# Performance work log

Measured on AMD Instinct MI355X. Metric: run time of the kernel, lower is better.

## Reference

```python
import jax, jax.numpy as jnp
import numpy as np
import math

S, B, D, H = 2048, 2, 1024, 16
HD = D // H  # head_dim = 64


def setup_inputs() -> dict:
    key = jax.random.key(0)
    ks = jax.random.split(key, 8)
    scale = 0.02
    return {
        "query": jax.random.normal(ks[0], (S, B, D), jnp.float32),
        "key": jax.random.normal(ks[1], (S, B, D), jnp.float32),
        "value": jax.random.normal(ks[2], (S, B, D), jnp.float32),
        "mask": jax.random.randint(ks[3], (1, S, 1, 1), 0, 2, jnp.int32),
        "w_q": jax.random.normal(ks[4], (D, D), jnp.float32) * scale,
        "b_q": jnp.zeros((D,), jnp.float32),
        "w_k": jax.random.normal(ks[5], (D, D), jnp.float32) * scale,
        "b_k": jnp.zeros((D,), jnp.float32),
        "w_v": jax.random.normal(ks[6], (D, D), jnp.float32) * scale,
        "b_v": jnp.zeros((D,), jnp.float32),
    }


def reference(query, key, value, mask, w_q, b_q, w_k, b_k, w_v, b_v):
    # Linear projections (torch Linear: x @ W^T + b); inputs are (S, B, D)
    q = query @ w_q.T + b_q
    k = key @ w_k.T + b_k
    v = value @ w_v.T + b_v
    # split heads: (S, B, H, HD)
    q = q.reshape(S, B, H, HD)
    k = k.reshape(S, B, H, HD)
    v = v.reshape(S, B, H, HD)
    # scores over (query_i, key_j, batch, head)
    scores = jnp.einsum("ibhd,jbhd->ijbh", q, k) * (1.0 / math.sqrt(HD))
    # mask (1, S, 1, 1) broadcasts against (i, j, b, h); 0 => masked
    scores = jnp.where(mask == 0, -jnp.inf, scores)
    # softmax over key axis j (original: nn.Softmax(dim=1))
    attn = jax.nn.softmax(scores, axis=1)
    out = jnp.einsum("ijbh,jbhd->ibhd", attn, v)  # (S, B, H, HD)
    return out.reshape(S, B, D)
```

## Files before the change

kernel.cpp:

```cpp
#include <hip/hip_runtime.h>
#include <stdint.h>


#define S_ 2048
#define B_ 2
#define D_ 1024
#define H_ 16
#define HD_ 64
#define M_ (S_ * B_)

typedef __bf16 bf16;
typedef bf16 bf16x8 __attribute__((ext_vector_type(8)));
typedef float floatx4 __attribute__((ext_vector_type(4)));

#define QSCALE 0.18033688011112042f

__device__ __forceinline__ void async_cp16(const bf16* g, bf16* l) {
    __builtin_amdgcn_global_load_lds(
        (const __attribute__((address_space(1))) void*)g,
        (__attribute__((address_space(3))) void*)l, 16, 0, 0);
}

#define TILE_OFF(bh, tile) (((size_t)(bh) * 32 + (tile)) * 4096)

__global__ __launch_bounds__(256) void mask_scan(const int* __restrict__ mask,
                                                 int* __restrict__ pos,
                                                 int* __restrict__ cnt)
{
    __shared__ int sums[256];
    const int tid = threadIdx.x;
    int v[8], s = 0;
    #pragma unroll
    for (int j = 0; j < 8; j++) { v[j] = mask[tid * 8 + j] ? 1 : 0; s += v[j]; }
    sums[tid] = s;
    __syncthreads();
    for (int off = 1; off < 256; off <<= 1) {
        int t = (tid >= off) ? sums[tid - off] : 0;
        __syncthreads();
        sums[tid] += t;
        __syncthreads();
    }
    int base = (tid > 0) ? sums[tid - 1] : 0;
    #pragma unroll
    for (int j = 0; j < 8; j++) { pos[tid * 8 + j] = base; base += v[j]; }
    if (tid == 255) cnt[0] = sums[255];
}

__global__ __launch_bounds__(256) void cvt6(
    const float* __restrict__ x0, const float* __restrict__ x1, const float* __restrict__ x2,
    const float* __restrict__ w0, const float* __restrict__ w1, const float* __restrict__ w2,
    bf16* __restrict__ o0, bf16* __restrict__ o1, bf16* __restrict__ o2,
    bf16* __restrict__ o3, bf16* __restrict__ o4, bf16* __restrict__ o5)
{
    const int z = blockIdx.y;
    if (z >= 3 && blockIdx.x >= 512) return;
    const float* src = (z == 0) ? x0 : (z == 1) ? x1 : (z == 2) ? x2
                     : (z == 3) ? w0 : (z == 4) ? w1 : w2;
    bf16* dst = (z == 0) ? o0 : (z == 1) ? o1 : (z == 2) ? o2
              : (z == 3) ? o3 : (z == 4) ? o4 : o5;
    const size_t i = ((size_t)blockIdx.x * 256 + threadIdx.x) * 8;
    floatx4 a = *(const floatx4*)(src + i);
    floatx4 b = *(const floatx4*)(src + i + 4);
    bf16x8 v;
    #pragma unroll
    for (int j = 0; j < 4; j++) { v[j] = (bf16)a[j]; v[4 + j] = (bf16)b[j]; }
    *(bf16x8*)(dst + i) = v;
}

#define TM 128
#define TN 64
#define BK 32

__global__ __launch_bounds__(256, 4) void qkv_gemm_async(
    const bf16* __restrict__ xq, const bf16* __restrict__ xk, const bf16* __restrict__ xv,
    const bf16* __restrict__ wq, const bf16* __restrict__ wk, const bf16* __restrict__ wv,
    const float* __restrict__ bq, const float* __restrict__ bk, const float* __restrict__ bv,
    const int* __restrict__ mask, const int* __restrict__ pos,
    bf16* __restrict__ oq, bf16* __restrict__ ok, bf16* __restrict__ ov)
{
    __shared__ __align__(16) bf16 a_lds[TM * BK];
    __shared__ __align__(16) bf16 b_lds[TN * BK];

    const int fid = blockIdx.x;
    const int xcd = fid & 7;
    const int t   = fid >> 3;
    const int z   = t >> 6;
    const int u   = t & 63;
    const int m0  = ((u & 3) * 8 + xcd) * TM;
    const int n0  = (u >> 2) * TN;

    const bf16*  X  = (z == 0) ? xq : (z == 1) ? xk : xv;
    const bf16*  W  = (z == 0) ? wq : (z == 1) ? wk : wv;
    const float* Bi = (z == 0) ? bq : (z == 1) ? bk : bv;

    const int tid  = threadIdx.x;
    const int wid  = tid >> 6;
    const int lane = tid & 63;
    const int wm = wid >> 1, wn = wid & 1;
    const int lm = lane & 15, lq = lane >> 4;
    const int ksw = lq ^ ((lm >> 1) & 3);

    floatx4 acc[4][2] = {};

    for (int kt = 0; kt < D_; kt += BK) {
        __syncthreads();
        #pragma unroll
        for (int tt = 0; tt < 2; tt++) {
            const int cb = (tt * 4 + wid) * 64;
            const int c  = cb + lane;
            const int row = c >> 2, kc = (c & 3) ^ ((c >> 3) & 3);
            async_cp16(X + (size_t)(m0 + row) * D_ + kt + kc * 8, a_lds + cb * 8);
        }
        {
            const int cb = wid * 64;
            const int c  = cb + lane;
            const int row = c >> 2, kc = (c & 3) ^ ((c >> 3) & 3);
            async_cp16(W + (size_t)(n0 + row) * D_ + kt + kc * 8, b_lds + cb * 8);
        }
        __syncthreads();

        bf16x8 af[4], bf[2];
        #pragma unroll
        for (int i = 0; i < 4; i++)
            af[i] = *(const bf16x8*)(a_lds + (wm * 64 + i * 16 + lm) * 32 + ksw * 8);
        #pragma unroll
        for (int j = 0; j < 2; j++)
            bf[j] = *(const bf16x8*)(b_lds + (wn * 32 + j * 16 + lm) * 32 + ksw * 8);
        #pragma unroll
        for (int i = 0; i < 4; i++)
            #pragma unroll
            for (int j = 0; j < 2; j++)
                acc[i][j] = __builtin_amdgcn_mfma_f32_16x16x32_bf16(
                    af[i], bf[j], acc[i][j], 0, 0, 0);
    }

    #pragma unroll
    for (int j = 0; j < 2; j++) {
        const int n = n0 + wn * 32 + j * 16 + lm;
        const float bias = Bi[n];
        const int h = n >> 6, hd = n & 63;
        #pragma unroll
        for (int i = 0; i < 4; i++) {
            const int mb = m0 + wm * 64 + i * 16 + lq * 4;
            #pragma unroll
            for (int r = 0; r < 4; r++) {
                const int m = mb + r;
                const int s = m >> 1, b = m & 1;
                const float v = acc[i][j][r] + bias;
                const int bh = b * H_ + h;
                if (z == 0) {
                    oq[((size_t)bh * S_ + s) * HD_ + hd] = (bf16)(v * QSCALE);
                } else if (mask[s]) {
                    const int cs = pos[s];
                    if (z == 1) {
                        ok[TILE_OFF(bh, cs >> 6) + (hd >> 3) * 512 +
                           (cs & 63) * 8 + (hd & 7)] = (bf16)v;
                    } else {
                        ov[TILE_OFF(bh, cs >> 6) + ((cs >> 3) & 7) * 512 +
                           hd * 8 + (cs & 7)] = (bf16)v;
                    }
                }
            }
        }
    }
}

__global__ __launch_bounds__(256, 4) void attn_kernel(
    const bf16* __restrict__ qw, const bf16* __restrict__ kw, const bf16* __restrict__ vtw,
    const int* __restrict__ cnt, float* __restrict__ out)
{
    __shared__ __align__(16) bf16 p_lds[4 * 16 * 72];

    const int fid  = blockIdx.x;
    const int xcd  = fid & 7;
    const int t    = fid >> 3;
    const int bh   = (t & 3) * 8 + xcd;
    const int q0   = (t >> 2) * 64;

    const int tid  = threadIdx.x;
    const int wid  = tid >> 6;
    const int lane = tid & 63;
    const int lm = lane & 15, lq = lane >> 4;
    const int count = cnt[0];
    const int ntiles = (count + 63) >> 6;

    bf16x8 qf[2];
    {
        const bf16* qp = qw + ((size_t)bh * S_ + q0 + wid * 16 + lm) * HD_;
        qf[0] = *(const bf16x8*)(qp + lq * 8);
        qf[1] = *(const bf16x8*)(qp + 32 + lq * 8);
    }

    float lsum[4] = {0.f, 0.f, 0.f, 0.f};
    floatx4 oacc[4] = {};
    bf16* pw = p_lds + wid * 16 * 72;

    for (int tl = 0; tl < ntiles; tl++) {
        const size_t tbase = TILE_OFF(bh, tl);
        const size_t foff  = (size_t)lq * 512 + (size_t)lm * 8;

        bf16x8 kf[2][4];
        #pragma unroll
        for (int ks = 0; ks < 2; ks++)
            #pragma unroll
            for (int n = 0; n < 4; n++)
                kf[ks][n] = *(const bf16x8*)(kw + tbase + ks * 2048 + foff + n * 128);

        floatx4 sacc[4] = {};
        #pragma unroll
        for (int ks = 0; ks < 2; ks++)
            #pragma unroll
            for (int n = 0; n < 4; n++)
                sacc[n] = __builtin_amdgcn_mfma_f32_16x16x32_bf16(
                    qf[ks], kf[ks][n], sacc[n], 0, 0, 0);

        const int jb = tl * 64;
        float valf[4];
        #pragma unroll
        for (int n = 0; n < 4; n++)
            valf[n] = (jb + n * 16 + lm < count) ? 1.0f : 0.0f;
        #pragma unroll
        for (int r = 0; r < 4; r++)
            #pragma unroll
            for (int n = 0; n < 4; n++) {
                const float p = exp2f(sacc[n][r]) * valf[n];
                lsum[r] += p;
                sacc[n][r] = p;
            }

        bf16x8 vf[2][4];
        #pragma unroll
        for (int ks = 0; ks < 2; ks++)
            #pragma unroll
            for (int n = 0; n < 4; n++)
                vf[ks][n] = *(const bf16x8*)(vtw + tbase + ks * 2048 + foff + n * 128);

        #pragma unroll
        for (int r = 0; r < 4; r++)
            #pragma unroll
            for (int n = 0; n < 4; n++)
                pw[(lq * 4 + r) * 72 + n * 16 + lm] = (bf16)sacc[n][r];

        #pragma unroll
        for (int ks = 0; ks < 2; ks++) {
            bf16x8 pf = *(const bf16x8*)(pw + lm * 72 + ks * 32 + lq * 8);
            #pragma unroll
            for (int n = 0; n < 4; n++)
                oacc[n] = __builtin_amdgcn_mfma_f32_16x16x32_bf16(
                    pf, vf[ks][n], oacc[n], 0, 0, 0);
        }
    }

    float invl[4];
    #pragma unroll
    for (int r = 0; r < 4; r++) {
        float lr = lsum[r];
        lr += __shfl_xor(lr, 1);
        lr += __shfl_xor(lr, 2);
        lr += __shfl_xor(lr, 4);
        lr += __shfl_xor(lr, 8);
        invl[r] = 1.0f / lr;
    }
    const int b = bh >> 4, h = bh & 15;
    #pragma unroll
    for (int n = 0; n < 4; n++)
        #pragma unroll
        for (int r = 0; r < 4; r++) {
            const int q = q0 + wid * 16 + lq * 4 + r;
            out[((size_t)q * B_ + b) * D_ + h * 64 + n * 16 + lm] = oacc[n][r] * invl[r];
        }
}

extern "C" void kernel_launch(void* const* d_in, const int* in_sizes, int n_in,
                              void* d_out, int out_size, void* d_ws, size_t ws_size,
                              hipStream_t stream) {
    const float* xq = (const float*)d_in[0];
    const float* xk = (const float*)d_in[1];
    const float* xv = (const float*)d_in[2];
    const int*  mask = (const int*)d_in[3];
    const float* wq = (const float*)d_in[4];
    const float* bq = (const float*)d_in[5];
    const float* wk = (const float*)d_in[6];
    const float* bk = (const float*)d_in[7];
    const float* wv = (const float*)d_in[8];
    const float* bv = (const float*)d_in[9];

    const size_t NX = (size_t)M_ * D_;
    const size_t NW = (size_t)D_ * D_;
    char* ws = (char*)d_ws;
    int* cnt = (int*)ws;
    int* pos = cnt + 16;
    char* base = ws + 16384;

    bf16* xqb = (bf16*)base;
    bf16* xkb = xqb + NX;
    bf16* xvb = xkb + NX;
    bf16* wqb = xvb + NX;
    bf16* wkb = wqb + NW;
    bf16* wvb = wkb + NW;
    bf16* q_ws  = wvb + NW;
    bf16* k_ws  = q_ws + NX;
    bf16* vt_ws = k_ws + NX;

    mask_scan<<<1, 256, 0, stream>>>(mask, pos, cnt);
    cvt6<<<dim3(2048, 6), 256, 0, stream>>>(xq, xk, xv, wq, wk, wv,
                                            xqb, xkb, xvb, wqb, wkb, wvb);
    qkv_gemm_async<<<1536, 256, 0, stream>>>(xqb, xkb, xvb, wqb, wkb, wvb,
                                             bq, bk, bv, mask, pos,
                                             q_ws, k_ws, vt_ws);
    attn_kernel<<<1024, 256, 0, stream>>>(q_ws, k_ws, vt_ws, cnt, (float*)d_out);
}
```

Baseline: 211.2 us.

## Fuse fp32-to-bf16 conversion into QKV GEMM with register prefetch and larger N tile

Removes the separate conversion kernel and has the QKV GEMM read fp32 inputs and weights directly, converting to bf16 in registers before storing to LDS. The next K-slice is prefetched into registers while the current slice is computed, replacing the async global-to-LDS copies. The N tile doubles to 128, halving the grid to 768 blocks, and occupancy hint drops to 3. This avoids writing and re-reading bf16 copies of all activations and weights, at the cost of reading twice as many bytes per GEMM load, higher register pressure, and synchronous LDS staging.

```diff
diff --git a/kernel.cpp b/kernel.cpp
--- a/kernel.cpp
+++ b/kernel.cpp
@@ -14,12 +14,6 @@
 typedef float floatx4 __attribute__((ext_vector_type(4)));
 
 #define QSCALE 0.18033688011112042f
-
-__device__ __forceinline__ void async_cp16(const bf16* g, bf16* l) {
-    __builtin_amdgcn_global_load_lds(
-        (const __attribute__((address_space(1))) void*)g,
-        (__attribute__((address_space(3))) void*)l, 16, 0, 0);
-}
 
 #define TILE_OFF(bh, tile) (((size_t)(bh) * 32 + (tile)) * 4096)
 
@@ -46,34 +40,13 @@
     if (tid == 255) cnt[0] = sums[255];
 }
 
-__global__ __launch_bounds__(256) void cvt6(
-    const float* __restrict__ x0, const float* __restrict__ x1, const float* __restrict__ x2,
-    const float* __restrict__ w0, const float* __restrict__ w1, const float* __restrict__ w2,
-    bf16* __restrict__ o0, bf16* __restrict__ o1, bf16* __restrict__ o2,
-    bf16* __restrict__ o3, bf16* __restrict__ o4, bf16* __restrict__ o5)
-{
-    const int z = blockIdx.y;
-    if (z >= 3 && blockIdx.x >= 512) return;
-    const float* src = (z == 0) ? x0 : (z == 1) ? x1 : (z == 2) ? x2
-                     : (z == 3) ? w0 : (z == 4) ? w1 : w2;
-    bf16* dst = (z == 0) ? o0 : (z == 1) ? o1 : (z == 2) ? o2
-              : (z == 3) ? o3 : (z == 4) ? o4 : o5;
-    const size_t i = ((size_t)blockIdx.x * 256 + threadIdx.x) * 8;
-    floatx4 a = *(const floatx4*)(src + i);
-    floatx4 b = *(const floatx4*)(src + i + 4);
-    bf16x8 v;
-    #pragma unroll
-    for (int j = 0; j < 4; j++) { v[j] = (bf16)a[j]; v[4 + j] = (bf16)b[j]; }
-    *(bf16x8*)(dst + i) = v;
-}
-
 #define TM 128
-#define TN 64
+#define TN 128
 #define BK 32
 
-__global__ __launch_bounds__(256, 4) void qkv_gemm_async(
-    const bf16* __restrict__ xq, const bf16* __restrict__ xk, const bf16* __restrict__ xv,
-    const bf16* __restrict__ wq, const bf16* __restrict__ wk, const bf16* __restrict__ wv,
+__global__ __launch_bounds__(256, 3) void qkv_gemm(
+    const float* __restrict__ xq, const float* __restrict__ xk, const float* __restrict__ xv,
+    const float* __restrict__ wq, const float* __restrict__ wk, const float* __restrict__ wv,
     const float* __restrict__ bq, const float* __restrict__ bk, const float* __restrict__ bv,
     const int* __restrict__ mask, const int* __restrict__ pos,
     bf16* __restrict__ oq, bf16* __restrict__ ok, bf16* __restrict__ ov)
@@ -84,13 +57,13 @@
     const int fid = blockIdx.x;
     const int xcd = fid & 7;
     const int t   = fid >> 3;
-    const int z   = t >> 6;
-    const int u   = t & 63;
+    const int z   = t >> 5;
+    const int u   = t & 31;
     const int m0  = ((u & 3) * 8 + xcd) * TM;
     const int n0  = (u >> 2) * TN;
 
-    const bf16*  X  = (z == 0) ? xq : (z == 1) ? xk : xv;
-    const bf16*  W  = (z == 0) ? wq : (z == 1) ? wk : wv;
+    const float* X  = (z == 0) ? xq : (z == 1) ? xk : xv;
+    const float* W  = (z == 0) ? wq : (z == 1) ? wk : wv;
     const float* Bi = (z == 0) ? bq : (z == 1) ? bk : bv;
 
     const int tid  = threadIdx.x;
@@ -100,43 +73,73 @@
     const int lm = lane & 15, lq = lane >> 4;
     const int ksw = lq ^ ((lm >> 1) & 3);
 
-    floatx4 acc[4][2] = {};
+    const int ca0 = tid, ca1 = tid + 256;
+    const size_t offA0 = (size_t)(m0 + (ca0 >> 2)) * D_ + (((ca0 & 3) ^ ((ca0 >> 3) & 3)) * 8);
+    const size_t offA1 = (size_t)(m0 + (ca1 >> 2)) * D_ + (((ca1 & 3) ^ ((ca1 >> 3) & 3)) * 8);
+    const size_t offB0 = (size_t)(n0 + (ca0 >> 2)) * D_ + (((ca0 & 3) ^ ((ca0 >> 3) & 3)) * 8);
+    const size_t offB1 = (size_t)(n0 + (ca1 >> 2)) * D_ + (((ca1 & 3) ^ ((ca1 >> 3) & 3)) * 8);
+
+    floatx4 pa[2][2], pb[2][2];
+
+    pa[0][0] = *(const floatx4*)(X + offA0);
+    pa[0][1] = *(const floatx4*)(X + offA0 + 4);
+    pa[1][0] = *(const floatx4*)(X + offA1);
+    pa[1][1] = *(const floatx4*)(X + offA1 + 4);
+    pb[0][0] = *(const floatx4*)(W + offB0);
+    pb[0][1] = *(const floatx4*)(W + offB0 + 4);
+    pb[1][0] = *(const floatx4*)(W + offB1);
+    pb[1][1] = *(const floatx4*)(W + offB1 + 4);
+
+    floatx4 acc[4][4] = {};
 
     for (int kt = 0; kt < D_; kt += BK) {
         __syncthreads();
-        #pragma unroll
-        for (int tt = 0; tt < 2; tt++) {
-            const int cb = (tt * 4 + wid) * 64;
-            const int c  = cb + lane;
-            const int row = c >> 2, kc = (c & 3) ^ ((c >> 3) & 3);
-            async_cp16(X + (size_t)(m0 + row) * D_ + kt + kc * 8, a_lds + cb * 8);
-        }
         {
-            const int cb = wid * 64;
-            const int c  = cb + lane;
-            const int row = c >> 2, kc = (c & 3) ^ ((c >> 3) & 3);
-            async_cp16(W + (size_t)(n0 + row) * D_ + kt + kc * 8, b_lds + cb * 8);
+            bf16x8 v0, v1, w0, w1;
+            #pragma unroll
+            for (int j = 0; j < 4; j++) {
+                v0[j] = (bf16)pa[0][0][j]; v0[4 + j] = (bf16)pa[0][1][j];
+                v1[j] = (bf16)pa[1][0][j]; v1[4 + j] = (bf16)pa[1][1][j];
+                w0[j] = (bf16)pb[0][0][j]; w0[4 + j] = (bf16)pb[0][1][j];
+                w1[j] = (bf16)pb[1][0][j]; w1[4 + j] = (bf16)pb[1][1][j];
+            }
+            *(bf16x8*)(a_lds + ca0 * 8) = v0;
+            *(bf16x8*)(a_lds + ca1 * 8) = v1;
+            *(bf16x8*)(b_lds + ca0 * 8) = w0;
+            *(bf16x8*)(b_lds + ca1 * 8) = w1;
         }
         __syncthreads();
 
-        bf16x8 af[4], bf[2];
+        if (kt + BK < D_) {
+            const int kn = kt + BK;
+            pa[0][0] = *(const floatx4*)(X + kn + offA0);
+            pa[0][1] = *(const floatx4*)(X + kn + offA0 + 4);
+            pa[1][0] = *(const floatx4*)(X + kn + offA1);
+            pa[1][1] = *(const floatx4*)(X + kn + offA1 + 4);
+            pb[0][0] = *(const floatx4*)(W + kn + offB0);
+            pb[0][1] = *(const floatx4*)(W + kn + offB0 + 4);
+            pb[1][0] = *(const floatx4*)(W + kn + offB1);
+            pb[1][1] = *(const floatx4*)(W + kn + offB1 + 4);
+        }
+
+        bf16x8 af[4], bfv[4];
         #pragma unroll
         for (int i = 0; i < 4; i++)
             af[i] = *(const bf16x8*)(a_lds + (wm * 64 + i * 16 + lm) * 32 + ksw * 8);
         #pragma unroll
-        for (int j = 0; j < 2; j++)
-            bf[j] = *(const bf16x8*)(b_lds + (wn * 32 + j * 16 + lm) * 32 + ksw * 8);
+        for (int j = 0; j < 4; j++)
+            bfv[j] = *(const bf16x8*)(b_lds + (wn * 64 + j * 16 + lm) * 32 + ksw * 8);
         #pragma unroll
         for (int i = 0; i < 4; i++)
             #pragma unroll
-            for (int j = 0; j < 2; j++)
+            for (int j = 0; j < 4; j++)
                 acc[i][j] = __builtin_amdgcn_mfma_f32_16x16x32_bf16(
-                    af[i], bf[j], acc[i][j], 0, 0, 0);
-    }
-
-    #pragma unroll
-    for (int j = 0; j < 2; j++) {
-        const int n = n0 + wn * 32 + j * 16 + lm;
+                    af[i], bfv[j], acc[i][j], 0, 0, 0);
+    }
+
+    #pragma unroll
+    for (int j = 0; j < 4; j++) {
+        const int n = n0 + wn * 64 + j * 16 + lm;
         const float bias = Bi[n];
         const int h = n >> 6, hd = n & 63;
         #pragma unroll
@@ -286,27 +289,18 @@
     const float* bv = (const float*)d_in[9];
 
     const size_t NX = (size_t)M_ * D_;
-    const size_t NW = (size_t)D_ * D_;
     char* ws = (char*)d_ws;
     int* cnt = (int*)ws;
     int* pos = cnt + 16;
     char* base = ws + 16384;
 
-    bf16* xqb = (bf16*)base;
-    bf16* xkb = xqb + NX;
-    bf16* xvb = xkb + NX;
-    bf16* wqb = xvb + NX;
-    bf16* wkb = wqb + NW;
-    bf16* wvb = wkb + NW;
-    bf16* q_ws  = wvb + NW;
+    bf16* q_ws  = (bf16*)base;
     bf16* k_ws  = q_ws + NX;
     bf16* vt_ws = k_ws + NX;
 
     mask_scan<<<1, 256, 0, stream>>>(mask, pos, cnt);
-    cvt6<<<dim3(2048, 6), 256, 0, stream>>>(xq, xk, xv, wq, wk, wv,
-                                            xqb, xkb, xvb, wqb, wkb, wvb);
-    qkv_gemm_async<<<1536, 256, 0, stream>>>(xqb, xkb, xvb, wqb, wkb, wvb,
-                                             bq, bk, bv, mask, pos,
-                                             q_ws, k_ws, vt_ws);
+    qkv_gemm<<<768, 256, 0, stream>>>(xq, xk, xv, wq, wk, wv,
+                                      bq, bk, bv, mask, pos,
+                                      q_ws, k_ws, vt_ws);
     attn_kernel<<<1024, 256, 0, stream>>>(q_ws, k_ws, vt_ws, cnt, (float*)d_out);
 }
```

Result: slower. 226.4 us (+7.2%).
